# Kernel tuning notes

Measured on AMD Instinct MI355X. Metric: run time of the kernel, lower is better.

## Reference

```python
import jax, jax.numpy as jnp
import numpy as np

VOCAB = 30522
BZ, SEQ, D, P = 32, 2048, 768, 16
PLACEHOLDER_ID = 1
UNK_ID = 100


def setup_inputs() -> dict:
    key = jax.random.key(0)
    k1, k2, k3, k4 = jax.random.split(key, 4)
    # random token ids, guaranteed != PLACEHOLDER_ID
    input_ids = jax.random.randint(k1, (BZ, SEQ), UNK_ID + 1, VOCAB)
    # choose exactly P distinct placeholder positions per row (module requires this)
    pos = jnp.argsort(jax.random.uniform(k2, (BZ, SEQ)), axis=1)[:, :P]
    input_ids = input_ids.at[jnp.arange(BZ)[:, None], pos].set(PLACEHOLDER_ID)
    emb_table = jax.random.normal(k3, (VOCAB, D), jnp.float32) * 0.02
    prompt = jax.random.normal(k4, (P, D), jnp.float32)
    return {"input_ids": input_ids, "emb_table": emb_table, "prompt": prompt}


def reference(input_ids, emb_table, prompt):
    # mask of placeholder positions; exactly P per row
    mask = input_ids == PLACEHOLDER_ID                         # [BZ, SEQ]
    # placeholder tokens are looked up as UNK, then overwritten by prompt rows
    emb = emb_table[jnp.where(mask, UNK_ID, input_ids)]        # [BZ, SEQ, D]
    # i-th placeholder (in sequence order) gets prompt[i] -> rank via cumsum
    rank = jnp.clip(jnp.cumsum(mask, axis=1) - 1, 0, P - 1)    # [BZ, SEQ]
    out = jnp.where(mask[:, :, None], prompt[rank], emb)       # [BZ, SEQ, D]
    return out
```

## Files before the change

### kernel.cpp

```cpp
#include <hip/hip_runtime.h>
#include <hip/hip_bf16.h>

#define VOCAB 30522
#define BZ 32
#define SEQ 2048
#define D 768
#define P 16
#define PLACEHOLDER_ID 1

__global__ void rank_kernel(const int* __restrict__ ids, int* __restrict__ rank) {
    const int b = blockIdx.x;
    const int t = threadIdx.x;
    constexpr int CHUNK = SEQ / 256;
    const int* row = ids + (size_t)b * SEQ;
    const int base = t * CHUNK;

    int m[CHUNK];
    int cnt = 0;
#pragma unroll
    for (int i = 0; i < CHUNK; ++i) {
        m[i] = (row[base + i] == PLACEHOLDER_ID) ? 1 : 0;
        cnt += m[i];
    }

    const int lane = t & 63;
    const int wave = t >> 6;
    int incl = cnt;
#pragma unroll
    for (int off = 1; off < 64; off <<= 1) {
        int v = __shfl_up(incl, off, 64);
        if (lane >= off) incl += v;
    }
    __shared__ int wsum[4];
    if (lane == 63) wsum[wave] = incl;
    __syncthreads();
    int woff = 0;
    for (int w = 0; w < wave; ++w) woff += wsum[w];

    int run = woff + (incl - cnt);
    int* rrow = rank + (size_t)b * SEQ;
#pragma unroll
    for (int i = 0; i < CHUNK; ++i) {
        run += m[i];
        int r = run - 1;
        r = r < 0 ? 0 : (r > (P - 1) ? (P - 1) : r);
        rrow[base + i] = r;
    }
}

__global__ void gather_kernel(const int* __restrict__ ids,
                              const float* __restrict__ emb,
                              const float* __restrict__ prompt,
                              const int* __restrict__ rank,
                              float* __restrict__ out) {
    const int row = blockIdx.x;
    const int id = ids[row];
    const float4* src;
    if (id == PLACEHOLDER_ID) {
        src = (const float4*)(prompt + (size_t)rank[row] * D);
    } else {
        src = (const float4*)(emb + (size_t)id * D);
    }
    float4* dst = (float4*)(out + (size_t)row * D);
    dst[threadIdx.x] = src[threadIdx.x];
}

extern "C" void kernel_launch(void* const* d_in, const int* in_sizes, int n_in,
                              void* d_out, int out_size, void* d_ws, size_t ws_size,
                              hipStream_t stream) {
    const int*   ids    = (const int*)d_in[0];
    const float* emb    = (const float*)d_in[1];
    const float* prompt = (const float*)d_in[2];
    float*       out    = (float*)d_out;
    int*         rank   = (int*)d_ws;

    rank_kernel<<<BZ, 256, 0, stream>>>(ids, rank);
    gather_kernel<<<BZ * SEQ, D / 4, 0, stream>>>(ids, emb, prompt, rank, out);
}
```

Measured before the change: 67.13 us.

## Batch 16 rows per gather block with batched loads and nontemporal stores

The gather kernel now copies 16 output rows per 256-thread block instead of one row per 192-thread block. Row source pointers are resolved once into shared memory, and each thread issues all of its 12 vector loads before its stores. Stores use nontemporal hints so the write-once output does not pollute cache. This cuts block-launch overhead and raises memory-level parallelism, at the cost of a shared-memory sync and more registers per thread.

```diff
diff --git a/kernel.cpp b/kernel.cpp
--- a/kernel.cpp
+++ b/kernel.cpp
@@ -7,6 +7,8 @@
 #define D 768
 #define P 16
 #define PLACEHOLDER_ID 1
+
+typedef float f32x4 __attribute__((ext_vector_type(4)));
 
 __global__ void rank_kernel(const int* __restrict__ ids, int* __restrict__ rank) {
     const int b = blockIdx.x;
@@ -48,21 +50,43 @@
     }
 }
 
-__global__ void gather_kernel(const int* __restrict__ ids,
-                              const float* __restrict__ emb,
-                              const float* __restrict__ prompt,
-                              const int* __restrict__ rank,
-                              float* __restrict__ out) {
-    const int row = blockIdx.x;
-    const int id = ids[row];
-    const float4* src;
-    if (id == PLACEHOLDER_ID) {
-        src = (const float4*)(prompt + (size_t)rank[row] * D);
-    } else {
-        src = (const float4*)(emb + (size_t)id * D);
+#define ROWS_PER_BLOCK 16
+__global__ __launch_bounds__(256) void gather_kernel(
+        const int* __restrict__ ids,
+        const float* __restrict__ emb,
+        const float* __restrict__ prompt,
+        const int* __restrict__ rank,
+        float* __restrict__ out) {
+    constexpr int NF4 = D / 4;
+    constexpr int F4_PER_BLOCK = ROWS_PER_BLOCK * NF4;
+    constexpr int ITERS = F4_PER_BLOCK / 256;
+
+    const int t = threadIdx.x;
+    const int row0 = blockIdx.x * ROWS_PER_BLOCK;
+
+    __shared__ const f32x4* srcs[ROWS_PER_BLOCK];
+    if (t < ROWS_PER_BLOCK) {
+        const int id = ids[row0 + t];
+        srcs[t] = (id == PLACEHOLDER_ID)
+                      ? (const f32x4*)(prompt + (size_t)rank[row0 + t] * D)
+                      : (const f32x4*)(emb + (size_t)id * D);
     }
-    float4* dst = (float4*)(out + (size_t)row * D);
-    dst[threadIdx.x] = src[threadIdx.x];
+    __syncthreads();
+
+    f32x4* dst = (f32x4*)(out + (size_t)row0 * D);
+
+    f32x4 v[ITERS];
+#pragma unroll
+    for (int k = 0; k < ITERS; ++k) {
+        const int f = k * 256 + t;
+        const int r = f / NF4;
+        const int c = f - r * NF4;
+        v[k] = srcs[r][c];
+    }
+#pragma unroll
+    for (int k = 0; k < ITERS; ++k) {
+        __builtin_nontemporal_store(v[k], &dst[k * 256 + t]);
+    }
 }
 
 extern "C" void kernel_launch(void* const* d_in, const int* in_sizes, int n_in,
@@ -75,5 +99,6 @@
     int*         rank   = (int*)d_ws;
 
     rank_kernel<<<BZ, 256, 0, stream>>>(ids, rank);
-    gather_kernel<<<BZ * SEQ, D / 4, 0, stream>>>(ids, emb, prompt, rank, out);
+    gather_kernel<<<(BZ * SEQ) / ROWS_PER_BLOCK, 256, 0, stream>>>(
+        ids, emb, prompt, rank, out);
 }
```

New measurement: 67.01 us. About the same (-0.2%).
